# Optimization experiments

Hardware: AMD Instinct MI355X
Metric: run time of the kernel (lower is better)

## Reference

```python
import jax, jax.numpy as jnp
import numpy as np


def setup_inputs() -> dict:
    key = jax.random.key(0)
    k1, k2, k3, k4, k5 = jax.random.split(key, 5)
    B, Te, Td, De, Dd = 8, 256, 256, 512, 512
    return {
        "encoder_out_seq": jax.random.normal(k1, (B, Te, De), dtype=jnp.float32),
        "decoder_out_seq": jax.random.normal(k2, (B, Td, Dd), dtype=jnp.float32),
        "W_a": jax.random.normal(k3, (De, De), dtype=jnp.float32) * 0.05,
        "U_a": jax.random.normal(k4, (Dd, De), dtype=jnp.float32) * 0.05,
        "V_a": jax.random.normal(k5, (De, 1), dtype=jnp.float32) * 0.05,
    }


def reference(encoder_out_seq, decoder_out_seq, W_a, U_a, V_a):
    # Bahdanau additive attention, fully vectorized over decoder timesteps
    # (replaces the two sequential K.rnn scans in the original).
    Ws = jnp.einsum('bte,ef->btf', encoder_out_seq, W_a)   # [B,Te,De]
    Uh = jnp.einsum('bqd,df->bqf', decoder_out_seq, U_a)   # [B,Td,De]
    # scores[b,q,t] = tanh(Ws[b,t,:] + Uh[b,q,:]) . V_a
    scores = jnp.einsum('bqtf,f->bqt',
                        jnp.tanh(Ws[:, None, :, :] + Uh[:, :, None, :]),
                        V_a[:, 0])                          # [B,Td,Te]
    e = jax.nn.softmax(scores, axis=-1)                     # attention weights
    c = jnp.einsum('bqt,btf->bqf', e, encoder_out_seq)      # context vectors
    return (c, e)
```

## Files before the change

### kernel.cpp

```cpp
#include <hip/hip_runtime.h>

#define NB 8
#define TE 256
#define TD 256
#define DE 512
#define QT 4

#define K2SCALE 2.8853900817779268f

typedef short bf16x8 __attribute__((ext_vector_type(8)));
typedef float f32x4 __attribute__((ext_vector_type(4)));
typedef unsigned short u16x8 __attribute__((ext_vector_type(8)));

static __device__ __forceinline__ unsigned short f2bf(float x) {
  unsigned int u = __float_as_uint(x);
  u += 0x7fffu + ((u >> 16) & 1u);
  return (unsigned short)(u >> 16);
}

static __device__ __forceinline__ void split8(
    const float4& x0, const float4& x1, u16x8& h, u16x8& l) {
  float xs[8] = {x0.x, x0.y, x0.z, x0.w, x1.x, x1.y, x1.z, x1.w};
  #pragma unroll
  for (int j = 0; j < 8; ++j) {
    unsigned int u = __float_as_uint(xs[j]);
    h[j] = (unsigned short)(u >> 16);
    float hf = __uint_as_float(u & 0xffff0000u);
    l[j] = f2bf(xs[j] - hf);
  }
}

__global__ __launch_bounds__(256) void convB(
    const float* __restrict__ w0, unsigned short* __restrict__ h0, unsigned short* __restrict__ l0,
    const float* __restrict__ w1, unsigned short* __restrict__ h1, unsigned short* __restrict__ l1)
{
  const float* W = blockIdx.z ? w1 : w0;
  unsigned short* H = blockIdx.z ? h1 : h0;
  unsigned short* L = blockIdx.z ? l1 : l0;
  __shared__ unsigned short sh[32][33], sl[32][33];
  const int t = threadIdx.x;
  const int k0 = blockIdx.y * 32, n0 = blockIdx.x * 32;
  const int r = t >> 3, c = (t & 7) * 4;
  float4 x = *(const float4*)(W + (size_t)(k0 + r) * DE + n0 + c);
  float xs[4] = {x.x, x.y, x.z, x.w};
  #pragma unroll
  for (int j = 0; j < 4; ++j) {
    unsigned short hh = f2bf(xs[j]);
    float hf = __uint_as_float((unsigned int)hh << 16);
    sh[r][c + j] = hh;
    sl[r][c + j] = f2bf(xs[j] - hf);
  }
  __syncthreads();
  ushort4 oh, ol;
  oh.x = sh[c + 0][r]; oh.y = sh[c + 1][r]; oh.z = sh[c + 2][r]; oh.w = sh[c + 3][r];
  ol.x = sl[c + 0][r]; ol.y = sl[c + 1][r]; ol.z = sl[c + 2][r]; ol.w = sl[c + 3][r];
  *(ushort4*)(H + (size_t)(n0 + r) * DE + k0 + c) = oh;
  *(ushort4*)(L + (size_t)(n0 + r) * DE + k0 + c) = ol;
}

__global__ __launch_bounds__(256) void gemm_mfma(
    const float* __restrict__ A0,
    const unsigned short* __restrict__ BH0, const unsigned short* __restrict__ BL0,
    float* __restrict__ C0,
    const float* __restrict__ A1,
    const unsigned short* __restrict__ BH1, const unsigned short* __restrict__ BL1,
    float* __restrict__ C1)
{
  const float*          A  = blockIdx.z ? A1  : A0;
  const unsigned short* BH = blockIdx.z ? BH1 : BH0;
  const unsigned short* BL = blockIdx.z ? BL1 : BL0;
  float*                C  = blockIdx.z ? C1  : C0;
  const int tid  = threadIdx.x;
  const int lane = tid & 63;
  const int wave = tid >> 6;
  const int wm = wave >> 1, wn = wave & 1;
  const int g = lane >> 4, r16 = lane & 15;
  const int m0 = blockIdx.y * 128, n0 = blockIdx.x * 64;
  __shared__ __align__(16) unsigned short Ah[2][128][40], Al[2][128][40];
  __shared__ __align__(16) unsigned short Bh[2][64][40],  Bl[2][64][40];
  const int arow = tid >> 2;
  const int apart = (tid & 3) * 8;

  float4 a00, a01, a10, a11;
  u16x8 pb, plb;
#define LOADTILE(KT) do {                                                   \
    const size_t ko = (size_t)(KT) * 32 + apart;                            \
    const float* pa_ = A + (size_t)(m0 + arow) * 512 + ko;                  \
    a00 = *(const float4*)pa_;       a01 = *(const float4*)(pa_ + 4);       \
    a10 = *(const float4*)(pa_ + 64 * 512);                                 \
    a11 = *(const float4*)(pa_ + 64 * 512 + 4);                             \
    pb  = *(const u16x8*)(BH + (size_t)(n0 + arow) * 512 + ko);             \
    plb = *(const u16x8*)(BL + (size_t)(n0 + arow) * 512 + ko);             \
  } while (0)
#define STORETILE(BUF) do {                                                 \
    u16x8 h0_, l0_, h1_, l1_;                                               \
    split8(a00, a01, h0_, l0_);                                             \
    split8(a10, a11, h1_, l1_);                                             \
    *(u16x8*)&Ah[BUF][arow][apart] = h0_;                                   \
    *(u16x8*)&Ah[BUF][arow + 64][apart] = h1_;                              \
    *(u16x8*)&Al[BUF][arow][apart] = l0_;                                   \
    *(u16x8*)&Al[BUF][arow + 64][apart] = l1_;                              \
    *(u16x8*)&Bh[BUF][arow][apart] = pb;                                    \
    *(u16x8*)&Bl[BUF][arow][apart] = plb;                                   \
  } while (0)

  f32x4 accm[4][2], acce[4][2];
  #pragma unroll
  for (int mt = 0; mt < 4; ++mt)
    #pragma unroll
    for (int nt = 0; nt < 2; ++nt) {
      accm[mt][nt] = (f32x4){0.f, 0.f, 0.f, 0.f};
      acce[mt][nt] = (f32x4){0.f, 0.f, 0.f, 0.f};
    }

  LOADTILE(0);
  STORETILE(0);
  __syncthreads();

  for (int kt = 0; kt < 16; ++kt) {
    const int cur = kt & 1;
    if (kt + 1 < 16) LOADTILE(kt + 1);
    bf16x8 ah[4], al[4], bh[2], bl[2];
    #pragma unroll
    for (int mt = 0; mt < 4; ++mt) {
      ah[mt] = *(const bf16x8*)&Ah[cur][wm * 64 + mt * 16 + r16][g * 8];
      al[mt] = *(const bf16x8*)&Al[cur][wm * 64 + mt * 16 + r16][g * 8];
    }
    #pragma unroll
    for (int nt = 0; nt < 2; ++nt) {
      bh[nt] = *(const bf16x8*)&Bh[cur][wn * 32 + nt * 16 + r16][g * 8];
      bl[nt] = *(const bf16x8*)&Bl[cur][wn * 32 + nt * 16 + r16][g * 8];
    }
    #pragma unroll
    for (int mt = 0; mt < 4; ++mt)
      #pragma unroll
      for (int nt = 0; nt < 2; ++nt) {
        accm[mt][nt] = __builtin_amdgcn_mfma_f32_16x16x32_bf16(ah[mt], bh[nt], accm[mt][nt], 0, 0, 0);
        acce[mt][nt] = __builtin_amdgcn_mfma_f32_16x16x32_bf16(al[mt], bh[nt], acce[mt][nt], 0, 0, 0);
        acce[mt][nt] = __builtin_amdgcn_mfma_f32_16x16x32_bf16(ah[mt], bl[nt], acce[mt][nt], 0, 0, 0);
      }
    if (kt + 1 < 16) STORETILE(cur ^ 1);
    __syncthreads();
  }
#undef LOADTILE
#undef STORETILE

  #pragma unroll
  for (int mt = 0; mt < 4; ++mt)
    #pragma unroll
    for (int nt = 0; nt < 2; ++nt)
      #pragma unroll
      for (int j = 0; j < 4; ++j) {
        float vsum = accm[mt][nt][j] + acce[mt][nt][j];
        int row = m0 + wm * 64 + mt * 16 + g * 4 + j;
        int col = n0 + wn * 32 + nt * 16 + r16;
        C[(size_t)row * 512 + col] = __builtin_amdgcn_exp2f(vsum * K2SCALE);
      }
}

__global__ __launch_bounds__(512) void attn(
    const float* __restrict__ ws, const float* __restrict__ uh,
    const float* __restrict__ enc, const float* __restrict__ va,
    float* __restrict__ out_c, float* __restrict__ out_e)
{
  const int tid  = threadIdx.x;
  const int wave = tid >> 6;
  const int lane = tid & 63;
  const int b  = blockIdx.x >> 6;
  const int q0 = (blockIdx.x & 63) * QT;
  __shared__ float s_sc[QT][TE];
  __shared__ float red[3][QT][DE];
  const int fbase = lane * 8;

  float4 v0 = *(const float4*)(va + fbase);
  float4 v1 = *(const float4*)(va + fbase + 4);
  float v[8] = {v0.x, v0.y, v0.z, v0.w, v1.x, v1.y, v1.z, v1.w};

  float eu[QT][8];
  #pragma unroll
  for (int q = 0; q < QT; ++q) {
    const float* up = uh + (size_t)(b * TD + q0 + q) * DE + fbase;
    float4 u0 = *(const float4*)(up);
    float4 u1 = *(const float4*)(up + 4);
    eu[q][0] = u0.x; eu[q][1] = u0.y; eu[q][2] = u0.z; eu[q][3] = u0.w;
    eu[q][4] = u1.x; eu[q][5] = u1.y; eu[q][6] = u1.z; eu[q][7] = u1.w;
  }

  const int t0 = wave * 32;
  const float* wp = ws + (size_t)(b * TE + t0) * DE + fbase;
  float4 w0 = *(const float4*)(wp);
  float4 w1 = *(const float4*)(wp + 4);
  for (int t = t0; t < t0 + 32; ++t) {
    float cw[8] = {w0.x, w0.y, w0.z, w0.w, w1.x, w1.y, w1.z, w1.w};
    wp += DE;
    w0 = *(const float4*)(wp);
    w1 = *(const float4*)(wp + 4);
    float a[QT];
    #pragma unroll
    for (int q = 0; q < QT; ++q) {
      float A0 = fmaf(cw[0], eu[q][0], 1.f);
      float A1 = fmaf(cw[1], eu[q][1], 1.f);
      float A2 = fmaf(cw[2], eu[q][2], 1.f);
      float A3 = fmaf(cw[3], eu[q][3], 1.f);
      float B0 = fmaf(cw[4], eu[q][4], 1.f);
      float B1 = fmaf(cw[5], eu[q][5], 1.f);
      float B2 = fmaf(cw[6], eu[q][6], 1.f);
      float B3 = fmaf(cw[7], eu[q][7], 1.f);
      float n1 = fmaf(v[1], A0, v[0] * A1);
      float d1 = A0 * A1;
      float n2 = fmaf(v[3], A2, v[2] * A3);
      float d2 = A2 * A3;
      float N1 = fmaf(n2, d1, n1 * d2);
      float D1 = d1 * d2;
      float n3 = fmaf(v[5], B0, v[4] * B1);
      float d3 = B0 * B1;
      float n4 = fmaf(v[7], B2, v[6] * B3);
      float d4 = B2 * B3;
      float N2 = fmaf(n4, d3, n3 * d4);
      float D2 = d3 * d4;
      float s = N1 * __builtin_amdgcn_rcpf(D1);
      a[q] = fmaf(N2, __builtin_amdgcn_rcpf(D2), s);
    }
    {
      const bool h1 = lane & 1;
      float m0 = h1 ? a[1] : a[0], o0 = h1 ? a[0] : a[1];
      float m1 = h1 ? a[3] : a[2], o1 = h1 ? a[2] : a[3];
      float r0 = m0 + __shfl_xor(o0, 1, 64);
      float r1 = m1 + __shfl_xor(o1, 1, 64);
      const bool h2 = lane & 2;
      float mm = h2 ? r1 : r0, oo = h2 ? r0 : r1;
      float r = mm + __shfl_xor(oo, 2, 64);
      r += __shfl_xor(r, 4, 64);
      r += __shfl_xor(r, 8, 64);
      r += __shfl_xor(r, 16, 64);
      r += __shfl_xor(r, 32, 64);
      if (lane < QT) s_sc[lane][t] = -2.f * r;
    }
  }
  __syncthreads();

  if (wave < QT) {
    const int r = wave;
    float x[4];
    #pragma unroll
    for (int i = 0; i < 4; ++i) x[i] = s_sc[r][lane + 64 * i];
    float m = fmaxf(fmaxf(x[0], x[1]), fmaxf(x[2], x[3]));
    #pragma unroll
    for (int off = 32; off >= 1; off >>= 1) m = fmaxf(m, __shfl_xor(m, off, 64));
    const float L2E = 1.4426950408889634f;
    float ssum = 0.f;
    #pragma unroll
    for (int i = 0; i < 4; ++i) { x[i] = __builtin_amdgcn_exp2f((x[i] - m) * L2E); ssum += x[i]; }
    #pragma unroll
    for (int off = 32; off >= 1; off >>= 1) ssum += __shfl_xor(ssum, off, 64);
    float inv = 1.f / ssum;
    float* oe = out_e + (size_t)(b * TD + q0 + r) * TE;
    #pragma unroll
    for (int i = 0; i < 4; ++i) {
      float e = x[i] * inv;
      s_sc[r][lane + 64 * i] = e;
      oe[lane + 64 * i] = e;
    }
  }
  __syncthreads();

  {
    const int fgrp = tid >> 7;
    const int f4   = (tid & 127) * 4;
    float4 c[QT];
    #pragma unroll
    for (int q = 0; q < QT; ++q) c[q] = make_float4(0.f, 0.f, 0.f, 0.f);
    const float* eb = enc + (size_t)b * TE * DE + f4;
    const int tb = fgrp * 64;
    #pragma unroll 4
    for (int t = tb; t < tb + 64; ++t) {
      float4 ee = *(const float4*)(eb + (size_t)t * DE);
      #pragma unroll
      for (int q = 0; q < QT; ++q) {
        float w = s_sc[q][t];
        c[q].x = fmaf(w, ee.x, c[q].x);
        c[q].y = fmaf(w, ee.y, c[q].y);
        c[q].z = fmaf(w, ee.z, c[q].z);
        c[q].w = fmaf(w, ee.w, c[q].w);
      }
    }
    if (fgrp > 0) {
      #pragma unroll
      for (int q = 0; q < QT; ++q) *(float4*)&red[fgrp - 1][q][f4] = c[q];
    }
    __syncthreads();
    if (fgrp == 0) {
      #pragma unroll
      for (int q = 0; q < QT; ++q) {
        float4 r1 = *(const float4*)&red[0][q][f4];
        float4 r2 = *(const float4*)&red[1][q][f4];
        float4 r3 = *(const float4*)&red[2][q][f4];
        c[q].x += (r1.x + r2.x) + r3.x;
        c[q].y += (r1.y + r2.y) + r3.y;
        c[q].z += (r1.z + r2.z) + r3.z;
        c[q].w += (r1.w + r2.w) + r3.w;
        *(float4*)(out_c + (size_t)(b * TD + q0 + q) * DE + f4) = c[q];
      }
    }
  }
}

extern "C" void kernel_launch(void* const* d_in, const int* in_sizes, int n_in,
                              void* d_out, int out_size, void* d_ws, size_t ws_size,
                              hipStream_t stream) {
  const float* enc = (const float*)d_in[0];
  const float* dec = (const float*)d_in[1];
  const float* Wa  = (const float*)d_in[2];
  const float* Ua  = (const float*)d_in[3];
  const float* Va  = (const float*)d_in[4];
  float* out_c = (float*)d_out;
  float* out_e = out_c + (size_t)NB * TD * DE;

  float* ws = (float*)d_ws;
  float* uh = ws + 1048576;
  unsigned short* BHw = (unsigned short*)(uh + 1048576);
  unsigned short* BLw = BHw + 262144;
  unsigned short* BHu = BLw + 262144;
  unsigned short* BLu = BHu + 262144;

  convB<<<dim3(16, 16, 2), dim3(256), 0, stream>>>(Wa, BHw, BLw, Ua, BHu, BLu);
  gemm_mfma<<<dim3(8, 16, 2), dim3(256), 0, stream>>>(
      enc, BHw, BLw, ws, dec, BHu, BLu, uh);
  attn<<<dim3(NB * (TD / QT)), dim3(512), 0, stream>>>(
      ws, uh, enc, Va, out_c, out_e);
}
```

Before: 72.09 us.

## Shrink GEMM tiles, remap blocks per XCD, reorder attention batches

The GEMM tile shrinks from 128x64 to 64x64 and the grid becomes a flat 512 blocks instead of 256. Each block index is remapped so that blocks landing on the same XCD share an A row panel, for better L2 reuse. The attention kernel now interleaves the batch index across consecutive blocks, so the same batch's data spreads across XCDs rather than clustering. The split8 high part now uses round-to-nearest instead of truncation, which slightly changes precision. In exchange there is less MFMA work per block and more redundant B loads.

```diff
diff --git a/kernel.cpp b/kernel.cpp
--- a/kernel.cpp
+++ b/kernel.cpp
@@ -23,9 +23,9 @@
   float xs[8] = {x0.x, x0.y, x0.z, x0.w, x1.x, x1.y, x1.z, x1.w};
   #pragma unroll
   for (int j = 0; j < 8; ++j) {
-    unsigned int u = __float_as_uint(xs[j]);
-    h[j] = (unsigned short)(u >> 16);
-    float hf = __uint_as_float(u & 0xffff0000u);
+    unsigned short hh = f2bf(xs[j]);
+    float hf = __uint_as_float((unsigned int)hh << 16);
+    h[j] = hh;
     l[j] = f2bf(xs[j] - hf);
   }
 }
@@ -66,47 +66,49 @@
     const unsigned short* __restrict__ BH1, const unsigned short* __restrict__ BL1,
     float* __restrict__ C1)
 {
-  const float*          A  = blockIdx.z ? A1  : A0;
-  const unsigned short* BH = blockIdx.z ? BH1 : BH0;
-  const unsigned short* BL = blockIdx.z ? BL1 : BL0;
-  float*                C  = blockIdx.z ? C1  : C0;
+  const int blk = blockIdx.x;
+  const int xcd = blk & 7;
+  const int j = blk >> 3;
+  const int panel = xcd * 8 + (j & 7);
+  const int bx = j >> 3;
+  const int by = panel & 31;
+  const int bz = panel >> 5;
+  const float*          A  = bz ? A1  : A0;
+  const unsigned short* BH = bz ? BH1 : BH0;
+  const unsigned short* BL = bz ? BL1 : BL0;
+  float*                C  = bz ? C1  : C0;
   const int tid  = threadIdx.x;
   const int lane = tid & 63;
   const int wave = tid >> 6;
   const int wm = wave >> 1, wn = wave & 1;
   const int g = lane >> 4, r16 = lane & 15;
-  const int m0 = blockIdx.y * 128, n0 = blockIdx.x * 64;
-  __shared__ __align__(16) unsigned short Ah[2][128][40], Al[2][128][40];
-  __shared__ __align__(16) unsigned short Bh[2][64][40],  Bl[2][64][40];
+  const int m0 = by * 64, n0 = bx * 64;
+  __shared__ __align__(16) unsigned short Ah[2][64][40], Al[2][64][40];
+  __shared__ __align__(16) unsigned short Bh[2][64][40], Bl[2][64][40];
   const int arow = tid >> 2;
   const int apart = (tid & 3) * 8;
 
-  float4 a00, a01, a10, a11;
+  float4 a00, a01;
   u16x8 pb, plb;
 #define LOADTILE(KT) do {                                                   \
     const size_t ko = (size_t)(KT) * 32 + apart;                            \
     const float* pa_ = A + (size_t)(m0 + arow) * 512 + ko;                  \
-    a00 = *(const float4*)pa_;       a01 = *(const float4*)(pa_ + 4);       \
-    a10 = *(const float4*)(pa_ + 64 * 512);                                 \
-    a11 = *(const float4*)(pa_ + 64 * 512 + 4);                             \
+    a00 = *(const float4*)pa_;  a01 = *(const float4*)(pa_ + 4);            \
     pb  = *(const u16x8*)(BH + (size_t)(n0 + arow) * 512 + ko);             \
     plb = *(const u16x8*)(BL + (size_t)(n0 + arow) * 512 + ko);             \
   } while (0)
 #define STORETILE(BUF) do {                                                 \
-    u16x8 h0_, l0_, h1_, l1_;                                               \
+    u16x8 h0_, l0_;                                                         \
     split8(a00, a01, h0_, l0_);                                             \
-    split8(a10, a11, h1_, l1_);                                             \
     *(u16x8*)&Ah[BUF][arow][apart] = h0_;                                   \
-    *(u16x8*)&Ah[BUF][arow + 64][apart] = h1_;                              \
     *(u16x8*)&Al[BUF][arow][apart] = l0_;                                   \
-    *(u16x8*)&Al[BUF][arow + 64][apart] = l1_;                              \
     *(u16x8*)&Bh[BUF][arow][apart] = pb;                                    \
     *(u16x8*)&Bl[BUF][arow][apart] = plb;                                   \
   } while (0)
 
-  f32x4 accm[4][2], acce[4][2];
-  #pragma unroll
-  for (int mt = 0; mt < 4; ++mt)
+  f32x4 accm[2][2], acce[2][2];
+  #pragma unroll
+  for (int mt = 0; mt < 2; ++mt)
     #pragma unroll
     for (int nt = 0; nt < 2; ++nt) {
       accm[mt][nt] = (f32x4){0.f, 0.f, 0.f, 0.f};
@@ -120,11 +122,11 @@
   for (int kt = 0; kt < 16; ++kt) {
     const int cur = kt & 1;
     if (kt + 1 < 16) LOADTILE(kt + 1);
-    bf16x8 ah[4], al[4], bh[2], bl[2];
-    #pragma unroll
-    for (int mt = 0; mt < 4; ++mt) {
-      ah[mt] = *(const bf16x8*)&Ah[cur][wm * 64 + mt * 16 + r16][g * 8];
-      al[mt] = *(const bf16x8*)&Al[cur][wm * 64 + mt * 16 + r16][g * 8];
+    bf16x8 ah[2], al[2], bh[2], bl[2];
+    #pragma unroll
+    for (int mt = 0; mt < 2; ++mt) {
+      ah[mt] = *(const bf16x8*)&Ah[cur][wm * 32 + mt * 16 + r16][g * 8];
+      al[mt] = *(const bf16x8*)&Al[cur][wm * 32 + mt * 16 + r16][g * 8];
     }
     #pragma unroll
     for (int nt = 0; nt < 2; ++nt) {
@@ -132,7 +134,7 @@
       bl[nt] = *(const bf16x8*)&Bl[cur][wn * 32 + nt * 16 + r16][g * 8];
     }
     #pragma unroll
-    for (int mt = 0; mt < 4; ++mt)
+    for (int mt = 0; mt < 2; ++mt)
       #pragma unroll
       for (int nt = 0; nt < 2; ++nt) {
         accm[mt][nt] = __builtin_amdgcn_mfma_f32_16x16x32_bf16(ah[mt], bh[nt], accm[mt][nt], 0, 0, 0);
@@ -146,13 +148,13 @@
 #undef STORETILE
 
   #pragma unroll
-  for (int mt = 0; mt < 4; ++mt)
+  for (int mt = 0; mt < 2; ++mt)
     #pragma unroll
     for (int nt = 0; nt < 2; ++nt)
       #pragma unroll
-      for (int j = 0; j < 4; ++j) {
-        float vsum = accm[mt][nt][j] + acce[mt][nt][j];
-        int row = m0 + wm * 64 + mt * 16 + g * 4 + j;
+      for (int jj = 0; jj < 4; ++jj) {
+        float vsum = accm[mt][nt][jj] + acce[mt][nt][jj];
+        int row = m0 + wm * 32 + mt * 16 + g * 4 + jj;
         int col = n0 + wn * 32 + nt * 16 + r16;
         C[(size_t)row * 512 + col] = __builtin_amdgcn_exp2f(vsum * K2SCALE);
       }
@@ -166,8 +168,8 @@
   const int tid  = threadIdx.x;
   const int wave = tid >> 6;
   const int lane = tid & 63;
-  const int b  = blockIdx.x >> 6;
-  const int q0 = (blockIdx.x & 63) * QT;
+  const int b  = blockIdx.x & 7;
+  const int q0 = (blockIdx.x >> 3) * QT;
   __shared__ float s_sc[QT][TE];
   __shared__ float red[3][QT][DE];
   const int fbase = lane * 8;
@@ -324,7 +326,7 @@
   unsigned short* BLu = BHu + 262144;
 
   convB<<<dim3(16, 16, 2), dim3(256), 0, stream>>>(Wa, BHw, BLw, Ua, BHu, BLu);
-  gemm_mfma<<<dim3(8, 16, 2), dim3(256), 0, stream>>>(
+  gemm_mfma<<<dim3(512), dim3(256), 0, stream>>>(
       enc, BHw, BLw, ws, dec, BHu, BLu, uh);
   attn<<<dim3(NB * (TD / QT)), dim3(512), 0, stream>>>(
       ws, uh, enc, Va, out_c, out_e);
```

After: 68.72 us. -4.7%, faster.
